# Kernel optimization log

Hardware: AMD Instinct MI355X
Metric: run time of the kernel (lower is better)

Reference implementation:

```python
import jax, jax.numpy as jnp
import numpy as np

D_MODEL = 1024
C = 128
BATCH = 4
SEQ = 2048


def setup_inputs() -> dict:
    key = jax.random.key(0)
    k1, k2, k3, k4, k5 = jax.random.split(key, 5)
    x = jax.random.normal(k1, (BATCH, SEQ, D_MODEL), dtype=jnp.float32)
    # init_param_ uses fan-based scaling; emulate with scaled normals
    A = jax.random.normal(k2, (D_MODEL, C), dtype=jnp.float32) / np.sqrt(D_MODEL)
    Bmat = jax.random.normal(k3, (C, D_MODEL), dtype=jnp.float32) / np.sqrt(C)
    ov = jax.random.normal(k4, (D_MODEL, D_MODEL), dtype=jnp.float32) / np.sqrt(D_MODEL)
    mask = jax.random.uniform(k5, (BATCH, SEQ, C), dtype=jnp.float32)
    return {"x": x, "A": A, "Bmat": Bmat, "ov": ov, "mask": mask}


def reference(x, A, Bmat, ov, mask):
    # query_acts: [b, s, C], key_acts: [b, s, C]
    q = jnp.einsum('bsd,dc->bsc', x, A)
    k = jnp.einsum('bsd,cd->bsc', x, Bmat)
    # masked per-channel score reduction:
    # sum_c (q[b,q,c] * k[b,k,c] * mask[b,q,c]) == (q*mask) @ k^T
    scores = jnp.einsum('bqc,bkc->bqk', q * mask, k) / D_MODEL  # attn_scores_normed=True
    seq = x.shape[1]
    causal = jnp.triu(jnp.ones((seq, seq), dtype=bool), k=1)
    scores = jnp.where(causal[None, :, :], -jnp.inf, scores)
    patt = jax.nn.softmax(scores, axis=-1)  # [b, seqQ, seqK]
    z = jnp.einsum('bqk,bkd->bqd', patt, x)
    out = jnp.einsum('bqd,de->bqe', z, ov)
    return out
```

## Files before the change

kernel.cpp:

```cpp
#include <hip/hip_runtime.h>
#include <hip/hip_bf16.h>
#include <math.h>

#define D_MODEL 1024
#define C_DIM   128
#define BATCH   4
#define SEQ     2048
#define BS_ROWS (BATCH*SEQ)

typedef float  f32x4 __attribute__((ext_vector_type(4)));
typedef short  s16x8 __attribute__((ext_vector_type(8)));
typedef unsigned short u16;
typedef unsigned short u16x4 __attribute__((ext_vector_type(4)));

__device__ inline u16 f2bf(float f){
    unsigned u = __builtin_bit_cast(unsigned, f);
    u += 0x7FFF + ((u >> 16) & 1);
    return (u16)(u >> 16);
}

__device__ inline void gl_lds16(const u16* g, u16* l){
    __builtin_amdgcn_global_load_lds(
        (const __attribute__((address_space(1))) void*)g,
        (__attribute__((address_space(3))) void*)l,
        16, 0, 0);
}

template<int N> __device__ inline void wait_vm(){
    if constexpr (N <= 0)      asm volatile("s_waitcnt vmcnt(0)" ::: "memory");
    else if constexpr (N == 4) asm volatile("s_waitcnt vmcnt(4)" ::: "memory");
    else if constexpr (N == 8) asm volatile("s_waitcnt vmcnt(8)" ::: "memory");
    else                       asm volatile("s_waitcnt vmcnt(0)" ::: "memory");
}

template<int BM, int BN, int WM, int WN, int OUT_BF16, int MASK, int CK,
         int EXPSUM, int RSCALE>
__device__ __forceinline__ void gemm_core(
    u16 (&As0)[BM*64], u16 (&As1)[BM*64],
    u16 (&Bs0)[BN*64], u16 (&Bs1)[BN*64],
    const u16* __restrict__ Aa, const u16* __restrict__ Bb,
    void* __restrict__ Cout, const float* __restrict__ mp,
    float* __restrict__ rowsum,
    int mt, int nt, int K, int lda, int ldb, int ldc, float scale)
{
    constexpr int W  = WM * WN;
    constexpr int PM = BM / WM, PN = BN / WN;
    constexpr int FM = PM / 16, FN = PN / 16;
    constexpr int CA = BM / 8 / W;
    constexpr int CB = BN / 8 / W;
    constexpr int NL = CA + CB;
    constexpr int ASZ = BM * 64, BSZ = BN * 64;

    const int tid = threadIdx.x, lane = tid & 63, wave = tid >> 6;
    const int wr = wave / WN, wc = wave % WN;
    const int mbase = mt * BM, nbase = nt * BN;
    int Keff = K;
    if (CK) { int ke = (mt + 1) * BM; Keff = ke < K ? ke : K; }
    const int nkt = Keff >> 6;

    f32x4 acc[FM][FN];
    #pragma unroll
    for (int m = 0; m < FM; ++m)
        #pragma unroll
        for (int n = 0; n < FN; ++n) acc[m][n] = (f32x4){0.f,0.f,0.f,0.f};

    const int sr  = lane >> 3;
    const int sc8 = (lane & 7) ^ sr;

    const u16* aptr[CA];
    const u16* bptr[CB];
    #pragma unroll
    for (int s = 0; s < CA; ++s)
        aptr[s] = Aa + (size_t)(mbase + (wave * CA + s) * 8 + sr) * lda + sc8 * 8;
    #pragma unroll
    for (int s = 0; s < CB; ++s)
        bptr[s] = Bb + (size_t)(nbase + (wave * CB + s) * 8 + sr) * ldb + sc8 * 8;

    auto STAGE = [&](u16 (&Ad)[ASZ], u16 (&Bd)[BSZ]) {
        #pragma unroll
        for (int s = 0; s < CA; ++s) { gl_lds16(aptr[s], &Ad[(wave * CA + s) * 512]); aptr[s] += 64; }
        #pragma unroll
        for (int s = 0; s < CB; ++s) { gl_lds16(bptr[s], &Bd[(wave * CB + s) * 512]); bptr[s] += 64; }
    };

    auto COMPUTE = [&](const u16 (&Ap)[ASZ], const u16 (&Bp)[BSZ]) {
        #pragma unroll
        for (int ks = 0; ks < 2; ++ks) {
            s16x8 af[FM], bfr[FN];
            const int k8 = ks * 4 + (lane >> 4);
            #pragma unroll
            for (int m = 0; m < FM; ++m) {
                const int row = wr * PM + m * 16 + (lane & 15);
                af[m] = *(const s16x8*)&Ap[row * 64 + ((k8 ^ (row & 7)) << 3)];
            }
            #pragma unroll
            for (int n = 0; n < FN; ++n) {
                const int row = wc * PN + n * 16 + (lane & 15);
                bfr[n] = *(const s16x8*)&Bp[row * 64 + ((k8 ^ (row & 7)) << 3)];
            }
            #pragma unroll
            for (int m = 0; m < FM; ++m)
                #pragma unroll
                for (int n = 0; n < FN; ++n)
                    acc[m][n] = __builtin_amdgcn_mfma_f32_16x16x32_bf16(af[m], bfr[n], acc[m][n], 0, 0, 0);
        }
    };

    STAGE(As0, Bs0);
    for (int t = 0; t < nkt; t += 2) {
        STAGE(As1, Bs1);
        wait_vm<NL>();
        __builtin_amdgcn_s_barrier();
        COMPUTE(As0, Bs0);
        __builtin_amdgcn_s_barrier();
        if (t + 2 < nkt) { STAGE(As0, Bs0); wait_vm<NL>(); }
        else             { wait_vm<0>(); }
        __builtin_amdgcn_s_barrier();
        COMPUTE(As1, Bs1);
        __builtin_amdgcn_s_barrier();
    }

    const int lr = (lane >> 4) * 4, lc = lane & 15;
    float rs[FM][4];
    if (EXPSUM) {
        #pragma unroll
        for (int m = 0; m < FM; ++m)
            #pragma unroll
            for (int r = 0; r < 4; ++r) rs[m][r] = 0.f;
    }
    #pragma unroll
    for (int m = 0; m < FM; ++m) {
        #pragma unroll
        for (int n = 0; n < FN; ++n) {
            const int gr = mbase + wr * PM + m * 16 + lr;
            const int gc = nbase + wc * PN + n * 16 + lc;
            #pragma unroll
            for (int r = 0; r < 4; ++r) {
                float f = acc[m][n][r] * scale;
                if (EXPSUM) {
                    f = (gc <= gr + r) ? __expf(f) : 0.f;
                    rs[m][r] += f;
                }
                if (RSCALE) f /= rowsum[gr + r];
                const size_t off = (size_t)(gr + r) * ldc + gc;
                if (MASK) { if (mp) f *= mp[off]; }
                if (OUT_BF16) ((u16*)Cout)[off] = f2bf(f);
                else          ((float*)Cout)[off] = f;
            }
        }
    }
    if (EXPSUM) {
        #pragma unroll
        for (int m = 0; m < FM; ++m) {
            #pragma unroll
            for (int r = 0; r < 4; ++r) {
                float v = rs[m][r];
                v += __shfl_xor(v, 1); v += __shfl_xor(v, 2);
                v += __shfl_xor(v, 4); v += __shfl_xor(v, 8);
                if ((lane & 15) == 0) {
                    const int gr = mbase + wr * PM + m * 16 + lr + r;
                    atomicAdd(rowsum + gr, v);
                }
            }
        }
    }
}

template<int BM, int BN, int WM, int WN, int OUT_BF16, int MASK, int CSKIP,
         int CK, int QKF, int EXPSUM, int RSCALE, int ORD, int PAIR>
__launch_bounds__(WM*WN*64)
__global__ void gemm_bt(const u16* __restrict__ Ag, const u16* __restrict__ Bg,
                        const u16* __restrict__ Bg2,
                        void* __restrict__ Cg, void* __restrict__ Cg2,
                        const float* __restrict__ maskp,
                        float* __restrict__ rowsum,
                        int gx, int gy,
                        int K, int lda, int ldb, int ldc,
                        long sA, long sB, long sC, float scale)
{
    constexpr int ASZ = BM * 64, BSZ = BN * 64;
    __shared__ u16 As0[ASZ];
    __shared__ u16 As1[ASZ];
    __shared__ u16 Bs0[BSZ];
    __shared__ u16 Bs1[BSZ];

    const int nwg = gridDim.x;
    const int l   = (blockIdx.x & 7) * (nwg >> 3) + (blockIdx.x >> 3);
    int mt, nt, z, path = 0;
    if (PAIR == 1) {
        const int pairid = l & 7;
        const int f      = (l >> 5) & 1;
        mt = f ? (gx - 1 - pairid) : pairid;
        const int ntz = ((l >> 3) & 3) | (((l >> 6) & 7) << 2);
        nt = ntz & 7;
        z  = ntz >> 3;
    } else if (ORD == 0) {
        mt = l % gx; const int r = l / gx; nt = r % gy; z = r / gy;
    } else {
        nt = l % gy; const int r = l / gy; mt = r % gx; z = r / gx;
    }
    if (QKF) { constexpr int NT = C_DIM / BN; path = nt / NT; nt = nt % NT; }
    if (CSKIP && nt * BN >= (mt + 1) * BM) return;

    const bool kpath = QKF && path;
    const u16* Aa = Ag + (long)z * sA;
    const u16* Bb = (kpath ? Bg2 : Bg) + (long)z * sB;
    void* CoutBase = kpath ? Cg2 : Cg;
    void* Cout = OUT_BF16 ? (void*)((u16*)CoutBase + (long)z * sC)
                          : (void*)((float*)CoutBase + (long)z * sC);
    const float* mp = (MASK && !kpath && maskp) ? maskp + (long)z * sC : nullptr;
    float* rsz = rowsum ? rowsum + (long)z * SEQ : nullptr;

    gemm_core<BM,BN,WM,WN,OUT_BF16,MASK,CK,EXPSUM,RSCALE>(
        As0, As1, Bs0, Bs1, Aa, Bb, Cout, mp, rsz,
        mt, nt, K, lda, ldb, ldc, scale);
}

__launch_bounds__(256)
__global__ void scores_xov_fused(const u16* __restrict__ qm,
                                 const u16* __restrict__ kk,
                                 u16* __restrict__ sc,
                                 float* __restrict__ rowsum,
                                 const u16* __restrict__ ovT,
                                 const u16* __restrict__ xb,
                                 u16* __restrict__ xovT)
{
    __shared__ u16 As0[128*64];
    __shared__ u16 As1[128*64];
    __shared__ u16 Bs0[128*64];
    __shared__ u16 Bs1[128*64];

    const int bid = blockIdx.x;
    if (bid < 512) {
        const int l = (bid & 7) * 64 + (bid >> 3);
        const int mt = l % 8;
        const int nt = l / 8;
        gemm_core<128,128,2,2, 1,0,0,0,0>(
            As0, As1, Bs0, Bs1,
            ovT, xb, xovT, nullptr, nullptr,
            mt, nt, D_MODEL, D_MODEL, D_MODEL, BS_ROWS, 1.0f);
    } else {
        const int sb = bid - 512;
        const int l = (sb & 7) * 128 + (sb >> 3);
        const int f = (l >> 5) & 1;
        const int p = (l & 31) | ((l >> 6) << 5);
        const int z = p >> 7;
        const int q = p & 127;
        const int mt = f ? 15 - (q & 15) : (q & 15);
        const int nt = f ? 15 - (q >> 4) : (q >> 4);
        if (nt > mt) return;
        gemm_core<128,128,2,2, 1,0,0,1,0>(
            As0, As1, Bs0, Bs1,
            qm + (long)z * SEQ * C_DIM,
            kk + (long)z * SEQ * C_DIM,
            sc + (long)z * SEQ * SEQ,
            nullptr,
            rowsum + (long)z * SEQ,
            mt, nt, C_DIM, C_DIM, C_DIM, SEQ, 1.0f / D_MODEL);
    }
}

__launch_bounds__(256)
__global__ void prep_all(const float* __restrict__ x,  u16* __restrict__ xb,
                         float* __restrict__ rowsum,
                         const float* __restrict__ Bm, u16* __restrict__ Bmb,
                         const float* __restrict__ ov, u16* __restrict__ ovT,
                         const float* __restrict__ A,  u16* __restrict__ AbT)
{
    __shared__ float t[32][33];
    const int bid = blockIdx.x;
    if (bid < 2048) {
        const int gid = bid * 256 + threadIdx.x;
        if (gid < BS_ROWS) rowsum[gid] = 0.f;
        const int n4 = BS_ROWS * D_MODEL / 4;
        for (int i = gid; i < n4; i += 2048 * 256) {
            float4 f = reinterpret_cast<const float4*>(x)[i];
            u16x4 o = { f2bf(f.x), f2bf(f.y), f2bf(f.z), f2bf(f.w) };
            reinterpret_cast<u16x4*>(xb)[i] = o;
        }
    } else if (bid < 2176) {
        const int gid = (bid - 2048) * 256 + threadIdx.x;
        float4 f = reinterpret_cast<const float4*>(Bm)[gid];
        u16x4 o = { f2bf(f.x), f2bf(f.y), f2bf(f.z), f2bf(f.w) };
        reinterpret_cast<u16x4*>(Bmb)[gid] = o;
    } else if (bid < 3200) {
        const int local = bid - 2176;
        const int c0 = (local & 31) * 32, r0 = (local >> 5) * 32;
        const int tx = threadIdx.x & 31, ty = threadIdx.x >> 5;
        #pragma unroll
        for (int i = 0; i < 32; i += 8)
            t[ty + i][tx] = ov[(size_t)(r0 + ty + i) * D_MODEL + c0 + tx];
        __syncthreads();
        #pragma unroll
        for (int i = 0; i < 32; i += 8)
            ovT[(size_t)(c0 + ty + i) * D_MODEL + r0 + tx] = f2bf(t[tx][ty + i]);
    } else {
        const int local = bid - 3200;
        const int c0 = (local & 3) * 32, r0 = (local >> 2) * 32;
        const int tx = threadIdx.x & 31, ty = threadIdx.x >> 5;
        #pragma unroll
        for (int i = 0; i < 32; i += 8)
            t[ty + i][tx] = A[(size_t)(r0 + ty + i) * C_DIM + c0 + tx];
        __syncthreads();
        #pragma unroll
        for (int i = 0; i < 32; i += 8)
            AbT[(size_t)(c0 + ty + i) * D_MODEL + r0 + tx] = f2bf(t[tx][ty + i]);
    }
}

extern "C" void kernel_launch(void* const* d_in, const int* in_sizes, int n_in,
                              void* d_out, int out_size, void* d_ws, size_t ws_size,
                              hipStream_t stream)
{
    const float* x    = (const float*)d_in[0];
    const float* A    = (const float*)d_in[1];
    const float* Bm   = (const float*)d_in[2];
    const float* ov   = (const float*)d_in[3];
    const float* mask = (const float*)d_in[4];

    char* w = (char*)d_ws;
    u16* xb   = (u16*)w; w += (size_t)BS_ROWS * D_MODEL * 2;
    u16* AbT  = (u16*)w; w += (size_t)C_DIM * D_MODEL * 2;
    u16* Bmb  = (u16*)w; w += (size_t)C_DIM * D_MODEL * 2;
    u16* ovT  = (u16*)w; w += (size_t)D_MODEL * D_MODEL * 2;
    u16* qm   = (u16*)w; w += (size_t)BS_ROWS * C_DIM * 2;
    u16* kk   = (u16*)w; w += (size_t)BS_ROWS * C_DIM * 2;
    u16* sc   = (u16*)w; w += (size_t)BATCH * SEQ * SEQ * 2;
    u16* xovT = (u16*)w; w += (size_t)D_MODEL * BS_ROWS * 2;
    float* rowsum = (float*)w; w += (size_t)BS_ROWS * 4;

    prep_all<<<3328, 256, 0, stream>>>(x, xb, rowsum, Bm, Bmb, ov, ovT, A, AbT);

    gemm_bt<64,64,2,2, 1,1,0,0,1,0,0, 1,0><<<512, 256, 0, stream>>>(
        xb, AbT, Bmb, qm, kk, mask, nullptr,
        128, 4,
        D_MODEL, D_MODEL, D_MODEL, C_DIM, 0, 0, 0, 1.0f);

    scores_xov_fused<<<1536, 256, 0, stream>>>(qm, kk, sc, rowsum, ovT, xb, xovT);

    gemm_bt<128,128,2,2, 0,0,0,1,0,0,1, 0,1><<<512, 256, 0, stream>>>(
        sc, xovT, nullptr, d_out, nullptr, nullptr, rowsum,
        16, 8,
        SEQ, SEQ, BS_ROWS, D_MODEL,
        (long)SEQ * SEQ, (long)SEQ , (long)SEQ * D_MODEL, 1.0f);
}
```

Before: 88.57 us.

## Split-K the causal output GEMM for long rows with atomic accumulation

The final softmax-times-xov GEMM is restructured. Output row tiles 8-15, which carry the longest causal K ranges, are split into two K chunks that accumulate with float atomicAdd into a zeroed output. Rows 0-7 keep a single direct-store path. The prep kernel gains blocks to zero the output, and the QK projection is moved into a dedicated kernel. This balances work across the 768 workgroups, at the cost of the extra zeroing writes and atomic traffic.

```diff
diff --git a/kernel.cpp b/kernel.cpp
--- a/kernel.cpp
+++ b/kernel.cpp
@@ -34,14 +34,15 @@
 }
 
 template<int BM, int BN, int WM, int WN, int OUT_BF16, int MASK, int CK,
-         int EXPSUM, int RSCALE>
+         int EXPSUM, int RSCALE, int ATOMIC>
 __device__ __forceinline__ void gemm_core(
     u16 (&As0)[BM*64], u16 (&As1)[BM*64],
     u16 (&Bs0)[BN*64], u16 (&Bs1)[BN*64],
     const u16* __restrict__ Aa, const u16* __restrict__ Bb,
     void* __restrict__ Cout, const float* __restrict__ mp,
     float* __restrict__ rowsum,
-    int mt, int nt, int K, int lda, int ldb, int ldc, float scale)
+    int mt, int nt, int K, int lda, int ldb, int ldc, float scale,
+    int kt0, int nktIn)
 {
     constexpr int W  = WM * WN;
     constexpr int PM = BM / WM, PN = BN / WN;
@@ -54,9 +55,13 @@
     const int tid = threadIdx.x, lane = tid & 63, wave = tid >> 6;
     const int wr = wave / WN, wc = wave % WN;
     const int mbase = mt * BM, nbase = nt * BN;
-    int Keff = K;
-    if (CK) { int ke = (mt + 1) * BM; Keff = ke < K ? ke : K; }
-    const int nkt = Keff >> 6;
+    int nkt;
+    if (nktIn > 0) nkt = nktIn;
+    else {
+        int Keff = K;
+        if (CK) { int ke = (mt + 1) * BM; Keff = ke < K ? ke : K; }
+        nkt = Keff >> 6;
+    }
 
     f32x4 acc[FM][FN];
     #pragma unroll
@@ -71,10 +76,10 @@
     const u16* bptr[CB];
     #pragma unroll
     for (int s = 0; s < CA; ++s)
-        aptr[s] = Aa + (size_t)(mbase + (wave * CA + s) * 8 + sr) * lda + sc8 * 8;
+        aptr[s] = Aa + (size_t)(mbase + (wave * CA + s) * 8 + sr) * lda + kt0 * 64 + sc8 * 8;
     #pragma unroll
     for (int s = 0; s < CB; ++s)
-        bptr[s] = Bb + (size_t)(nbase + (wave * CB + s) * 8 + sr) * ldb + sc8 * 8;
+        bptr[s] = Bb + (size_t)(nbase + (wave * CB + s) * 8 + sr) * ldb + kt0 * 64 + sc8 * 8;
 
     auto STAGE = [&](u16 (&Ad)[ASZ], u16 (&Bd)[BSZ]) {
         #pragma unroll
@@ -144,8 +149,9 @@
                 if (RSCALE) f /= rowsum[gr + r];
                 const size_t off = (size_t)(gr + r) * ldc + gc;
                 if (MASK) { if (mp) f *= mp[off]; }
-                if (OUT_BF16) ((u16*)Cout)[off] = f2bf(f);
-                else          ((float*)Cout)[off] = f;
+                if (ATOMIC)        atomicAdd(&((float*)Cout)[off], f);
+                else if (OUT_BF16) ((u16*)Cout)[off] = f2bf(f);
+                else               ((float*)Cout)[off] = f;
             }
         }
     }
@@ -166,54 +172,30 @@
     }
 }
 
-template<int BM, int BN, int WM, int WN, int OUT_BF16, int MASK, int CSKIP,
-         int CK, int QKF, int EXPSUM, int RSCALE, int ORD, int PAIR>
-__launch_bounds__(WM*WN*64)
-__global__ void gemm_bt(const u16* __restrict__ Ag, const u16* __restrict__ Bg,
-                        const u16* __restrict__ Bg2,
-                        void* __restrict__ Cg, void* __restrict__ Cg2,
-                        const float* __restrict__ maskp,
-                        float* __restrict__ rowsum,
-                        int gx, int gy,
-                        int K, int lda, int ldb, int ldc,
-                        long sA, long sB, long sC, float scale)
-{
-    constexpr int ASZ = BM * 64, BSZ = BN * 64;
-    __shared__ u16 As0[ASZ];
-    __shared__ u16 As1[ASZ];
-    __shared__ u16 Bs0[BSZ];
-    __shared__ u16 Bs1[BSZ];
+__launch_bounds__(256)
+__global__ void qk_proj(const u16* __restrict__ xb, const u16* __restrict__ AbT,
+                        const u16* __restrict__ Bmb,
+                        u16* __restrict__ qm, u16* __restrict__ kk,
+                        const float* __restrict__ maskp)
+{
+    __shared__ u16 As0[64*64];
+    __shared__ u16 As1[64*64];
+    __shared__ u16 Bs0[64*64];
+    __shared__ u16 Bs1[64*64];
 
     const int nwg = gridDim.x;
     const int l   = (blockIdx.x & 7) * (nwg >> 3) + (blockIdx.x >> 3);
-    int mt, nt, z, path = 0;
-    if (PAIR == 1) {
-        const int pairid = l & 7;
-        const int f      = (l >> 5) & 1;
-        mt = f ? (gx - 1 - pairid) : pairid;
-        const int ntz = ((l >> 3) & 3) | (((l >> 6) & 7) << 2);
-        nt = ntz & 7;
-        z  = ntz >> 3;
-    } else if (ORD == 0) {
-        mt = l % gx; const int r = l / gx; nt = r % gy; z = r / gy;
-    } else {
-        nt = l % gy; const int r = l / gy; mt = r % gx; z = r / gx;
-    }
-    if (QKF) { constexpr int NT = C_DIM / BN; path = nt / NT; nt = nt % NT; }
-    if (CSKIP && nt * BN >= (mt + 1) * BM) return;
-
-    const bool kpath = QKF && path;
-    const u16* Aa = Ag + (long)z * sA;
-    const u16* Bb = (kpath ? Bg2 : Bg) + (long)z * sB;
-    void* CoutBase = kpath ? Cg2 : Cg;
-    void* Cout = OUT_BF16 ? (void*)((u16*)CoutBase + (long)z * sC)
-                          : (void*)((float*)CoutBase + (long)z * sC);
-    const float* mp = (MASK && !kpath && maskp) ? maskp + (long)z * sC : nullptr;
-    float* rsz = rowsum ? rowsum + (long)z * SEQ : nullptr;
-
-    gemm_core<BM,BN,WM,WN,OUT_BF16,MASK,CK,EXPSUM,RSCALE>(
-        As0, As1, Bs0, Bs1, Aa, Bb, Cout, mp, rsz,
-        mt, nt, K, lda, ldb, ldc, scale);
+    const int nty = l % 4;
+    const int mt  = l / 4;
+    const int path = nty >> 1, nt = nty & 1;
+
+    const u16* Bb = path ? Bmb : AbT;
+    void* Cout = path ? (void*)kk : (void*)qm;
+    const float* mp = path ? nullptr : maskp;
+
+    gemm_core<64,64,2,2, 1,1,0,0,0,0>(
+        As0, As1, Bs0, Bs1, xb, Bb, Cout, mp, nullptr,
+        mt, nt, D_MODEL, D_MODEL, D_MODEL, C_DIM, 1.0f, 0, 0);
 }
 
 __launch_bounds__(256)
@@ -235,10 +217,10 @@
         const int l = (bid & 7) * 64 + (bid >> 3);
         const int mt = l % 8;
         const int nt = l / 8;
-        gemm_core<128,128,2,2, 1,0,0,0,0>(
+        gemm_core<128,128,2,2, 1,0,0,0,0,0>(
             As0, As1, Bs0, Bs1,
             ovT, xb, xovT, nullptr, nullptr,
-            mt, nt, D_MODEL, D_MODEL, D_MODEL, BS_ROWS, 1.0f);
+            mt, nt, D_MODEL, D_MODEL, D_MODEL, BS_ROWS, 1.0f, 0, 0);
     } else {
         const int sb = bid - 512;
         const int l = (sb & 7) * 128 + (sb >> 3);
@@ -249,14 +231,69 @@
         const int mt = f ? 15 - (q & 15) : (q & 15);
         const int nt = f ? 15 - (q >> 4) : (q >> 4);
         if (nt > mt) return;
-        gemm_core<128,128,2,2, 1,0,0,1,0>(
+        gemm_core<128,128,2,2, 1,0,0,1,0,0>(
             As0, As1, Bs0, Bs1,
             qm + (long)z * SEQ * C_DIM,
             kk + (long)z * SEQ * C_DIM,
             sc + (long)z * SEQ * SEQ,
             nullptr,
             rowsum + (long)z * SEQ,
-            mt, nt, C_DIM, C_DIM, C_DIM, SEQ, 1.0f / D_MODEL);
+            mt, nt, C_DIM, C_DIM, C_DIM, SEQ, 1.0f / D_MODEL, 0, 0);
+    }
+}
+
+__launch_bounds__(256)
+__global__ void outproj_split(const u16* __restrict__ sc,
+                              const u16* __restrict__ xovT,
+                              float* __restrict__ outp,
+                              const float* __restrict__ rowsum)
+{
+    __shared__ u16 As0[128*64];
+    __shared__ u16 As1[128*64];
+    __shared__ u16 Bs0[128*64];
+    __shared__ u16 Bs1[128*64];
+
+    const int nwg = gridDim.x;
+    const int l   = (blockIdx.x & 7) * (nwg >> 3) + (blockIdx.x >> 3);
+
+    int mt, nt, z, kt0, nktL, atomicPath;
+    if (l < 512) {
+        const int sid = l;
+        z = sid >> 7;
+        const int w = sid & 127;
+        mt = 15 - (w >> 4);
+        nt = (w >> 1) & 7;
+        const int ch = w & 1;
+        const int nkt = 2 * (mt + 1);
+        const int c0n = ((mt + 1) + 1) & ~1;
+        if (ch == 0) { kt0 = 0;   nktL = c0n; }
+        else         { kt0 = c0n; nktL = nkt - c0n; }
+        atomicPath = 1;
+    } else {
+        const int sid = l - 512;
+        z = sid >> 6;
+        const int w = sid & 63;
+        mt = 7 - (w >> 3);
+        nt = w & 7;
+        kt0 = 0; nktL = 2 * (mt + 1);
+        atomicPath = 0;
+    }
+
+    const u16* Aa = sc + (long)z * SEQ * SEQ;
+    const u16* Bb = xovT + (long)z * SEQ;
+    float* Cout = outp + (long)z * SEQ * D_MODEL;
+    float* rsz = (float*)(rowsum + (long)z * SEQ);
+
+    if (atomicPath) {
+        gemm_core<128,128,2,2, 0,0,0,0,1,1>(
+            As0, As1, Bs0, Bs1, Aa, Bb, Cout, nullptr, rsz,
+            mt, nt, SEQ, SEQ, BS_ROWS, D_MODEL, 1.0f,
+            kt0, nktL);
+    } else {
+        gemm_core<128,128,2,2, 0,0,0,0,1,0>(
+            As0, As1, Bs0, Bs1, Aa, Bb, Cout, nullptr, rsz,
+            mt, nt, SEQ, SEQ, BS_ROWS, D_MODEL, 1.0f,
+            kt0, nktL);
     }
 }
 
@@ -265,7 +302,8 @@
                          float* __restrict__ rowsum,
                          const float* __restrict__ Bm, u16* __restrict__ Bmb,
                          const float* __restrict__ ov, u16* __restrict__ ovT,
-                         const float* __restrict__ A,  u16* __restrict__ AbT)
+                         const float* __restrict__ A,  u16* __restrict__ AbT,
+                         float* __restrict__ outp)
 {
     __shared__ float t[32][33];
     const int bid = blockIdx.x;
@@ -294,7 +332,7 @@
         #pragma unroll
         for (int i = 0; i < 32; i += 8)
             ovT[(size_t)(c0 + ty + i) * D_MODEL + r0 + tx] = f2bf(t[tx][ty + i]);
-    } else {
+    } else if (bid < 3328) {
         const int local = bid - 3200;
         const int c0 = (local & 3) * 32, r0 = (local >> 2) * 32;
         const int tx = threadIdx.x & 31, ty = threadIdx.x >> 5;
@@ -305,6 +343,13 @@
         #pragma unroll
         for (int i = 0; i < 32; i += 8)
             AbT[(size_t)(c0 + ty + i) * D_MODEL + r0 + tx] = f2bf(t[tx][ty + i]);
+    } else {
+        const int gid = (bid - 3328) * 256 + threadIdx.x;
+        float4 zf = make_float4(0.f, 0.f, 0.f, 0.f);
+        float4* o4 = reinterpret_cast<float4*>(outp);
+        #pragma unroll
+        for (int i = 0; i < 4; ++i)
+            o4[(size_t)gid * 4 + i] = zf;
     }
 }
 
@@ -317,6 +362,7 @@
     const float* Bm   = (const float*)d_in[2];
     const float* ov   = (const float*)d_in[3];
     const float* mask = (const float*)d_in[4];
+    float* outp = (float*)d_out;
 
     char* w = (char*)d_ws;
     u16* xb   = (u16*)w; w += (size_t)BS_ROWS * D_MODEL * 2;
@@ -329,18 +375,11 @@
     u16* xovT = (u16*)w; w += (size_t)D_MODEL * BS_ROWS * 2;
     float* rowsum = (float*)w; w += (size_t)BS_ROWS * 4;
 
-    prep_all<<<3328, 256, 0, stream>>>(x, xb, rowsum, Bm, Bmb, ov, ovT, A, AbT);
-
-    gemm_bt<64,64,2,2, 1,1,0,0,1,0,0, 1,0><<<512, 256, 0, stream>>>(
-        xb, AbT, Bmb, qm, kk, mask, nullptr,
-        128, 4,
-        D_MODEL, D_MODEL, D_MODEL, C_DIM, 0, 0, 0, 1.0f);
+    prep_all<<<5376, 256, 0, stream>>>(x, xb, rowsum, Bm, Bmb, ov, ovT, A, AbT, outp);
+
+    qk_proj<<<512, 256, 0, stream>>>(xb, AbT, Bmb, qm, kk, mask);
 
     scores_xov_fused<<<1536, 256, 0, stream>>>(qm, kk, sc, rowsum, ovT, xb, xovT);
 
-    gemm_bt<128,128,2,2, 0,0,0,1,0,0,1, 0,1><<<512, 256, 0, stream>>>(
-        sc, xovT, nullptr, d_out, nullptr, nullptr, rowsum,
-        16, 8,
-        SEQ, SEQ, BS_ROWS, D_MODEL,
-        (long)SEQ * SEQ, (long)SEQ , (long)SEQ * D_MODEL, 1.0f);
-}
+    outproj_split<<<768, 256, 0, stream>>>(sc, xovT, outp, rowsum);
+}
```

New measurement: 109.6 us. 23.8% more time.
